# Kernel tuning notes

Hardware: AMD Instinct MI355X
Metric: run time of the kernel (lower is better)

The kernel has to match this reference:

```python
import jax, jax.numpy as jnp
import numpy as np
from jax import lax

B, S, H, T = 64, 512, 1024, 24


def setup_inputs() -> dict:
    key = jax.random.key(0)
    k1, k2, k3, k4, k5 = jax.random.split(key, 5)
    feats = jax.random.normal(k1, (B, S, H), dtype=jnp.float32)
    target = jax.random.randint(k2, (B, S), 0, T)  # tag ids (argmax of original one-hot target)
    # descending-sorted lengths -> prefix mask, matching the torch code's sorted-batch assumption
    lengths = jnp.sort(jax.random.randint(k3, (B,), S // 2, S + 1))[::-1]
    mask = jnp.arange(S)[None, :] < lengths[:, None]  # (B,S) bool
    # hidden2tag params (uniform init ~ nn.Linear default scale)
    bound = 1.0 / np.sqrt(H)
    W = jax.random.uniform(k4, (T, H), minval=-bound, maxval=bound, dtype=jnp.float32)
    b = jax.random.uniform(k5, (T,), minval=-bound, maxval=bound, dtype=jnp.float32)
    transition = jnp.zeros((T, T), dtype=jnp.float32)
    return {"feats": feats, "target": target, "mask": mask, "W": W, "b": b, "transition": transition}


def reference(feats, target, mask, W, b, transition):
    # emission scores: (B,S,T)
    emission = jnp.einsum("bsh,th->bst", feats, W) + b
    # gold path score
    sc = jnp.take_along_axis(emission, target[:, :, None], axis=2).squeeze(-1)  # (B,S)
    sc = sc.at[:, 1:].add(transition[target[:, :-1], target[:, 1:]])
    total_score = (sc * mask.astype(emission.dtype)).sum(axis=1)  # (B,)
    # forward algorithm (log-partition) as a scan over time
    p0 = emission[:, 0]  # (B,T)
    emis_t = jnp.swapaxes(emission[:, 1:], 0, 1)  # (S-1,B,T)
    mask_t = jnp.swapaxes(mask[:, 1:], 0, 1)      # (S-1,B)

    def step(p, xs):
        emit_i, m_i = xs
        # log_sum[b, prev, cur] = p[b, prev] + transition[prev, cur] + emit_i[b, cur]
        new_p = jax.nn.logsumexp(p[:, :, None] + transition[None, :, :] + emit_i[:, None, :], axis=1)
        return jnp.where(m_i[:, None], new_p, p), None

    p, _ = lax.scan(step, p0, (emis_t, mask_t))
    log_Z = jax.nn.logsumexp(p, axis=1)  # (B,)
    loss = -jnp.mean(total_score - log_Z)
    return loss, emission
```

## Files before the change

### kernel.cpp

```cpp
#include <hip/hip_runtime.h>
#include <cstdint>
#include <math.h>

#define B_ 64
#define S_ 512
#define H_ 1024
#define T_ 24

typedef unsigned int u32;
#define GLD_LDS16(g, l)                                                        \
    __builtin_amdgcn_global_load_lds(                                          \
        (const __attribute__((address_space(1))) u32*)(g),                     \
        (__attribute__((address_space(3))) u32*)(l), 16, 0, 0)

__device__ __forceinline__ float rl_f32(float x, int sl) {
    return __uint_as_float(__builtin_amdgcn_readlane(__float_as_uint(x), sl));
}

__global__ __launch_bounds__(512, 4) void gemm_kernel(const float* __restrict__ feats,
                                                      const float* __restrict__ W,
                                                      const float* __restrict__ bias,
                                                      float* __restrict__ emission) {
    __shared__ float4 tile4[2][1024];
    const int tid  = threadIdx.x;
    const int lane = tid & 63;
    const int w    = __builtin_amdgcn_readfirstlane(tid >> 6);
    const int t0   = w * 3;
    const long row0 = (long)blockIdx.x * 64;
    const float* fbase = feats + row0 * H_;

    float Wreg[3][16];
#pragma unroll
    for (int t = 0; t < 3; ++t) {
        const float* wr = W + (long)(t0 + t) * H_ + lane * 16;
#pragma unroll
        for (int m4 = 0; m4 < 4; ++m4) {
            const float4 v = *(const float4*)(wr + m4 * 4);
            Wreg[t][m4 * 4 + 0] = v.x;
            Wreg[t][m4 * 4 + 1] = v.y;
            Wreg[t][m4 * 4 + 2] = v.z;
            Wreg[t][m4 * 4 + 3] = v.w;
        }
    }

    const float* g0 = fbase + (long)lane * H_ + (2 * w) * 4;
    const float* g1 = g0 + 4;
#define STAGE(c, buf)                                                          \
    do {                                                                       \
        GLD_LDS16(g0 + (c) * 64, &tile4[(buf)][(2 * w) * 64]);                 \
        GLD_LDS16(g1 + (c) * 64, &tile4[(buf)][(2 * w + 1) * 64]);             \
    } while (0)

    float acc[3] = {0.f, 0.f, 0.f};
    STAGE(0, 0);

    for (int c = 0; c < 16; ++c) {
        __syncthreads();
        if (c + 1 < 16) STAGE(c + 1, (c + 1) & 1);
        const float4* tb = tile4[c & 1];
#pragma unroll
        for (int i = 0; i < 16; ++i) {
            const float4 fv = tb[i * 64 + lane];
            const int sl = 4 * c + (i >> 2);
            const int m = (i & 3) * 4;
#pragma unroll
            for (int t = 0; t < 3; ++t) {
                acc[t] = fmaf(fv.x, rl_f32(Wreg[t][m + 0], sl), acc[t]);
                acc[t] = fmaf(fv.y, rl_f32(Wreg[t][m + 1], sl), acc[t]);
                acc[t] = fmaf(fv.z, rl_f32(Wreg[t][m + 2], sl), acc[t]);
                acc[t] = fmaf(fv.w, rl_f32(Wreg[t][m + 3], sl), acc[t]);
            }
        }
    }

    float* out = emission + (row0 + lane) * T_ + t0;
#pragma unroll
    for (int t = 0; t < 3; ++t) out[t] = acc[t] + bias[t0 + t];
#undef STAGE
}

__global__ __launch_bounds__(64) void score_kernel(const float* __restrict__ emission,
                                                   const int* __restrict__ target,
                                                   const int* __restrict__ mask,
                                                   const float* __restrict__ trans,
                                                   float* __restrict__ ws_score) {
    const int b = blockIdx.x;
    const int lane = threadIdx.x;
    float sum = 0.f;
    for (int s = lane; s < S_; s += 64) {
        if (mask[b * S_ + s]) {
            const int tg = target[b * S_ + s];
            float v = emission[((long)b * S_ + s) * T_ + tg];
            if (s > 0) v += trans[target[b * S_ + s - 1] * T_ + tg];
            sum += v;
        }
    }
#pragma unroll
    for (int off = 32; off; off >>= 1) sum += __shfl_down(sum, off);
    if (lane == 0) ws_score[b] = sum;
}

#define DECL_E(i) const float E##i = __expf(trans[(i) * T_ + jj]);
#define FMA4(i0, i1, i2, i3)                                                   \
    s0 = fmaf(rl_f32(q, i0), E##i0, s0);                                       \
    s1 = fmaf(rl_f32(q, i1), E##i1, s1);                                       \
    s2 = fmaf(rl_f32(q, i2), E##i2, s2);                                       \
    s3 = fmaf(rl_f32(q, i3), E##i3, s3);

__global__ __launch_bounds__(64, 1) void scan_kernel(const float* __restrict__ emission,
                                                     const int* __restrict__ mask,
                                                     const float* __restrict__ trans,
                                                     float* __restrict__ ws_logZ) {
    const int b = blockIdx.x;
    const int j = threadIdx.x;
    const int jj = j < 24 ? j : 23;

    const float* em = emission + (long)b * S_ * T_;
    const int* mk = mask + b * S_;

    int mc = 0;
#pragma unroll
    for (int k = 0; k < 8; ++k) mc += mk[j + k * 64];
#pragma unroll
    for (int off = 32; off; off >>= 1) mc += __shfl_xor(mc, off);
    const int len = __builtin_amdgcn_readfirstlane(mc);

    DECL_E(0)  DECL_E(1)  DECL_E(2)  DECL_E(3)  DECL_E(4)  DECL_E(5)
    DECL_E(6)  DECL_E(7)  DECL_E(8)  DECL_E(9)  DECL_E(10) DECL_E(11)
    DECL_E(12) DECL_E(13) DECL_E(14) DECL_E(15) DECL_E(16) DECL_E(17)
    DECL_E(18) DECL_E(19) DECL_E(20) DECL_E(21) DECL_E(22) DECL_E(23)

    float q = (j < 24) ? __expf(em[j]) : 0.f;
    float C = 0.f;

    float lb[8];
#pragma unroll
    for (int k = 0; k < 8; ++k) lb[k] = em[(1 + k) * T_ + jj];

    for (int sb = 1; sb < S_; sb += 16) {
#pragma unroll
        for (int k = 0; k < 16; ++k) {
            const int s = sb + k;
            const float X = __expf(lb[k & 7]);
            const int sp = s + 8;
            lb[k & 7] = (sp < S_) ? em[sp * T_ + jj] : 0.f;

            if (s < len) {
                float s0 = 0.f, s1 = 0.f, s2 = 0.f, s3 = 0.f;
                FMA4(0, 1, 2, 3)
                FMA4(4, 5, 6, 7)
                FMA4(8, 9, 10, 11)
                FMA4(12, 13, 14, 15)
                FMA4(16, 17, 18, 19)
                FMA4(20, 21, 22, 23)
                q = ((s0 + s1) + (s2 + s3)) * X;
            }
        }
        const float r = rl_f32(q, 0);
        q *= (1.0f / r);
        C += __logf(r);
    }

    float ex = (j < 24) ? q : 0.f;
#pragma unroll
    for (int off = 32; off; off >>= 1) ex += __shfl_down(ex, off);
    if (j == 0) ws_logZ[b] = C + __logf(ex);
}

__global__ __launch_bounds__(64) void finalize_kernel(const float* __restrict__ ws_score,
                                                      const float* __restrict__ ws_logZ,
                                                      float* __restrict__ out) {
    const int l = threadIdx.x;
    float v = ws_score[l] - ws_logZ[l];
#pragma unroll
    for (int off = 32; off; off >>= 1) v += __shfl_down(v, off);
    if (l == 0) out[0] = -v * (1.0f / B_);
}

extern "C" void kernel_launch(void* const* d_in, const int* in_sizes, int n_in,
                              void* d_out, int out_size, void* d_ws, size_t ws_size,
                              hipStream_t stream) {
    const float* feats  = (const float*)d_in[0];
    const int*   target = (const int*)d_in[1];
    const int*   mask   = (const int*)d_in[2];
    const float* W      = (const float*)d_in[3];
    const float* bias   = (const float*)d_in[4];
    const float* trans  = (const float*)d_in[5];

    float* out = (float*)d_out;
    float* emission = out + 1;
    float* ws_score = (float*)d_ws;
    float* ws_logZ  = ws_score + 64;

    gemm_kernel<<<512, 512, 0, stream>>>(feats, W, bias, emission);
    score_kernel<<<64, 64, 0, stream>>>(emission, target, mask, trans, ws_score);
    scan_kernel<<<64, 64, 0, stream>>>(emission, mask, trans, ws_logZ);
    finalize_kernel<<<1, 64, 0, stream>>>(ws_score, ws_logZ, out);
}
```

Before: 307.3 us.

## Replace LDS-staged GEMM with direct per-row global loads in emission kernel

The emission GEMM no longer stages feature tiles into LDS via global_load_lds or broadcasts W through readlane. Each lane now streams its own feature row directly from global memory with float4 loads and a one-step prefetch, reading W rows as uniform loads. This removes LDS traffic, barriers and readlane overhead. The cost is that each lane's row access is strided by H across lanes (uncoalesced), and all 8 waves re-read the same feature row, relying on cache.

```diff
diff --git a/kernel.cpp b/kernel.cpp
--- a/kernel.cpp
+++ b/kernel.cpp
@@ -7,12 +7,6 @@
 #define H_ 1024
 #define T_ 24
 
-typedef unsigned int u32;
-#define GLD_LDS16(g, l)                                                        \
-    __builtin_amdgcn_global_load_lds(                                          \
-        (const __attribute__((address_space(1))) u32*)(g),                     \
-        (__attribute__((address_space(3))) u32*)(l), 16, 0, 0)
-
 __device__ __forceinline__ float rl_f32(float x, int sl) {
     return __uint_as_float(__builtin_amdgcn_readlane(__float_as_uint(x), sl));
 }
@@ -21,62 +15,44 @@
                                                       const float* __restrict__ W,
                                                       const float* __restrict__ bias,
                                                       float* __restrict__ emission) {
-    __shared__ float4 tile4[2][1024];
     const int tid  = threadIdx.x;
     const int lane = tid & 63;
     const int w    = __builtin_amdgcn_readfirstlane(tid >> 6);
     const int t0   = w * 3;
-    const long row0 = (long)blockIdx.x * 64;
-    const float* fbase = feats + row0 * H_;
+    const long row = (long)blockIdx.x * 64 + lane;
 
-    float Wreg[3][16];
-#pragma unroll
-    for (int t = 0; t < 3; ++t) {
-        const float* wr = W + (long)(t0 + t) * H_ + lane * 16;
-#pragma unroll
-        for (int m4 = 0; m4 < 4; ++m4) {
-            const float4 v = *(const float4*)(wr + m4 * 4);
-            Wreg[t][m4 * 4 + 0] = v.x;
-            Wreg[t][m4 * 4 + 1] = v.y;
-            Wreg[t][m4 * 4 + 2] = v.z;
-            Wreg[t][m4 * 4 + 3] = v.w;
-        }
+    const float* fr = feats + row * H_;
+    const float* w0 = W + (long)t0 * H_;
+    const float* w1 = w0 + H_;
+    const float* w2 = w1 + H_;
+
+    float a0 = 0.f, a1 = 0.f, a2 = 0.f;
+
+    float4 cur = *(const float4*)fr;
+#pragma unroll 4
+    for (int h = 0; h < H_; h += 4) {
+        float4 nxt;
+        if (h + 4 < H_) nxt = *(const float4*)(fr + h + 4);
+        else            nxt = float4{0.f, 0.f, 0.f, 0.f};
+
+        const float4 v0 = *(const float4*)(w0 + h);
+        const float4 v1 = *(const float4*)(w1 + h);
+        const float4 v2 = *(const float4*)(w2 + h);
+
+        a0 = fmaf(cur.x, v0.x, a0); a0 = fmaf(cur.y, v0.y, a0);
+        a0 = fmaf(cur.z, v0.z, a0); a0 = fmaf(cur.w, v0.w, a0);
+        a1 = fmaf(cur.x, v1.x, a1); a1 = fmaf(cur.y, v1.y, a1);
+        a1 = fmaf(cur.z, v1.z, a1); a1 = fmaf(cur.w, v1.w, a1);
+        a2 = fmaf(cur.x, v2.x, a2); a2 = fmaf(cur.y, v2.y, a2);
+        a2 = fmaf(cur.z, v2.z, a2); a2 = fmaf(cur.w, v2.w, a2);
+
+        cur = nxt;
     }
 
-    const float* g0 = fbase + (long)lane * H_ + (2 * w) * 4;
-    const float* g1 = g0 + 4;
-#define STAGE(c, buf)                                                          \
-    do {                                                                       \
-        GLD_LDS16(g0 + (c) * 64, &tile4[(buf)][(2 * w) * 64]);                 \
-        GLD_LDS16(g1 + (c) * 64, &tile4[(buf)][(2 * w + 1) * 64]);             \
-    } while (0)
-
-    float acc[3] = {0.f, 0.f, 0.f};
-    STAGE(0, 0);
-
-    for (int c = 0; c < 16; ++c) {
-        __syncthreads();
-        if (c + 1 < 16) STAGE(c + 1, (c + 1) & 1);
-        const float4* tb = tile4[c & 1];
-#pragma unroll
-        for (int i = 0; i < 16; ++i) {
-            const float4 fv = tb[i * 64 + lane];
-            const int sl = 4 * c + (i >> 2);
-            const int m = (i & 3) * 4;
-#pragma unroll
-            for (int t = 0; t < 3; ++t) {
-                acc[t] = fmaf(fv.x, rl_f32(Wreg[t][m + 0], sl), acc[t]);
-                acc[t] = fmaf(fv.y, rl_f32(Wreg[t][m + 1], sl), acc[t]);
-                acc[t] = fmaf(fv.z, rl_f32(Wreg[t][m + 2], sl), acc[t]);
-                acc[t] = fmaf(fv.w, rl_f32(Wreg[t][m + 3], sl), acc[t]);
-            }
-        }
-    }
-
-    float* out = emission + (row0 + lane) * T_ + t0;
-#pragma unroll
-    for (int t = 0; t < 3; ++t) out[t] = acc[t] + bias[t0 + t];
-#undef STAGE
+    float* out = emission + row * T_ + t0;
+    out[0] = a0 + bias[t0 + 0];
+    out[1] = a1 + bias[t0 + 1];
+    out[2] = a2 + bias[t0 + 2];
 }
 
 __global__ __launch_bounds__(64) void score_kernel(const float* __restrict__ emission,
```

Result: slower. 365.8 us (+19.1%).
